# Optimization experiments

Measured on AMD Instinct MI355X. Metric: run time of the kernel, lower is better.

## Reference

```python
import jax, jax.numpy as jnp
import numpy as np

N_ATOMS = 10000
N_EDGES = 200000
L_MAX = 2
K_L = [32, 24, 16]  # k_max_l = n_element_channels * n_max_l

# (l1, l2, L) in the original loop order (l1 outer, l2 inner, L ascending)
PAIRS = [(0,0,0),(0,1,1),(0,2,2),
         (1,0,1),(1,1,0),(1,1,1),(1,1,2),(1,2,1),(1,2,2),
         (2,0,2),(2,1,1),(2,1,2),(2,2,0),(2,2,1),(2,2,2)]
# concatenated input width -> k_max_l[L] per (L, sigma) channel
LIN = {'0_1': (72, 32), '1_1': (80, 24), '1_m1': (40, 24), '2_1': (72, 16), '2_m1': (32, 16)}


def setup_inputs() -> dict:
    key = jax.random.key(0)
    it = iter(jax.random.split(key, 64))
    def nrm(shape):
        return jax.random.normal(next(it), shape, dtype=jnp.float32)
    inp = {}
    for l in range(L_MAX + 1):
        inp['rb%d' % l] = nrm((N_EDGES, K_L[l]))           # radial basis per l
    for l in range(L_MAX + 1):
        inp['sh%d' % l] = nrm((N_EDGES, 2*l+1, 1))         # spherical harmonics per l
    inp['emb'] = nrm((N_ATOMS, 1, K_L[0]))                 # initial center embedding
    for l in range(L_MAX + 1):
        inp['f%d' % l] = nrm((N_ATOMS, 2*l+1, K_L[l]))     # nu=1 equivariant features
    for (l1, l2, L) in PAIRS:
        inp['cg_%d_%d_%d' % (l1, l2, L)] = nrm(((2*l1+1)*(2*l2+1), 2*L+1))
    for LS, (fin, fout) in LIN.items():
        inp['W_' + LS] = nrm((fin, fout)) / np.float32(np.sqrt(fin))
        inp['b_' + LS] = nrm((fout,)) * 0.01
    inp['centers'] = jax.random.randint(next(it), (N_EDGES,), 0, N_ATOMS)
    inp['neighbors'] = jax.random.randint(next(it), (N_EDGES,), 0, N_ATOMS)
    inp['n_atoms'] = N_ATOMS
    return inp


def _normalize(x, dims):
    # Normalizer(dims): RMS normalization over the given dims
    return x * jax.lax.rsqrt(jnp.mean(x * x, axis=dims, keepdims=True) + 1e-12)


def _forward(floats, centers, neighbors, n_atoms):
    (rb0, rb1, rb2, sh0, sh1, sh2, emb, f0, f1, f2,
     cg_0_0_0, cg_0_1_1, cg_0_2_2, cg_1_0_1, cg_1_1_0, cg_1_1_1, cg_1_1_2,
     cg_1_2_1, cg_1_2_2, cg_2_0_2, cg_2_1_1, cg_2_1_2, cg_2_2_0, cg_2_2_1,
     cg_2_2_2, W_0_1, b_0_1, W_1_1, b_1_1, W_1_m1, b_1_m1, W_2_1, b_2_1,
     W_2_m1, b_2_m1) = floats
    rb = [rb0, rb1, rb2]; sh = [sh0, sh1, sh2]; feats = [f0, f1, f2]
    cgs = {'0_0_0': cg_0_0_0, '0_1_1': cg_0_1_1, '0_2_2': cg_0_2_2,
           '1_0_1': cg_1_0_1, '1_1_0': cg_1_1_0, '1_1_1': cg_1_1_1,
           '1_1_2': cg_1_1_2, '1_2_1': cg_1_2_1, '1_2_2': cg_1_2_2,
           '2_0_2': cg_2_0_2, '2_1_1': cg_2_1_1, '2_1_2': cg_2_1_2,
           '2_2_0': cg_2_2_0, '2_2_1': cg_2_2_1, '2_2_2': cg_2_2_2}
    lin = {'0_1': (W_0_1, b_0_1), '1_1': (W_1_1, b_1_1), '1_m1': (W_1_m1, b_1_m1),
           '2_1': (W_2_1, b_2_1), '2_m1': (W_2_m1, b_2_m1)}

    # ---- InvariantMessagePasser: density_l = scatter_add over centers of
    #      sh_l * rb_l * emb[neighbors]
    emb_n = emb[neighbors]                                       # [E, 1, k0]
    densities = []
    for l in range(L_MAX + 1):
        msg = sh[l] * rb[l][:, None, :] * emb_n[:, :, :K_L[l]]   # [E, 2l+1, k_l]
        densities.append(jax.ops.segment_sum(msg, centers, num_segments=n_atoms))

    # ---- EquivariantMessagePasser
    ve = [sh[l] * rb[l][:, None, :] for l in range(L_MAX + 1)]   # vector expansion [E,2l+1,k_l]
    fn = [feats[l][neighbors] for l in range(L_MAX + 1)]         # gathered neighbor feats
    results = {}
    for (l1, l2, L) in PAIRS:
        S = (-1) ** (l1 + l2 + L)
        k = min(K_L[l1], K_L[l2])
        t1 = ve[l1][:, :, :k]                                    # [E, 2l1+1, k]
        t2 = fn[l2][:, :, :k]                                    # [E, 2l2+1, k]
        cg = cgs['%d_%d_%d' % (l1, l2, L)].reshape(2*l1+1, 2*l2+1, 2*L+1)
        # fused outer product + CG contraction -> [E, 2L+1, k]
        res = jnp.einsum('eak,ebk,abM->eMk', t1, t2, cg)
        pooled = jax.ops.segment_sum(res, centers, num_segments=n_atoms)
        LS = '%d_%s' % (L, 'm1' if S < 0 else '1')
        results.setdefault(LS, []).append(pooled)

    outs = {}
    for LS, (W, b) in lin.items():
        x = jnp.concatenate(results[LS], axis=2)                 # [n_atoms, 2L+1, size_LS]
        x = _normalize(x, (0, 1))
        x = jnp.einsum('amf,fk->amk', x, W) + b
        outs[LS] = _normalize(x, (0, 1, 2))

    return (densities[0], densities[1], densities[2],
            outs['0_1'], outs['1_1'], outs['1_m1'], outs['2_1'], outs['2_m1'])


def reference(rb0, rb1, rb2, sh0, sh1, sh2, emb, f0, f1, f2,
              cg_0_0_0, cg_0_1_1, cg_0_2_2, cg_1_0_1, cg_1_1_0, cg_1_1_1,
              cg_1_1_2, cg_1_2_1, cg_1_2_2, cg_2_0_2, cg_2_1_1, cg_2_1_2,
              cg_2_2_0, cg_2_2_1, cg_2_2_2, W_0_1, b_0_1, W_1_1, b_1_1,
              W_1_m1, b_1_m1, W_2_1, b_2_1, W_2_m1, b_2_m1,
              centers, neighbors, n_atoms):
    floats = (rb0, rb1, rb2, sh0, sh1, sh2, emb, f0, f1, f2,
              cg_0_0_0, cg_0_1_1, cg_0_2_2, cg_1_0_1, cg_1_1_0, cg_1_1_1,
              cg_1_1_2, cg_1_2_1, cg_1_2_2, cg_2_0_2, cg_2_1_1, cg_2_1_2,
              cg_2_2_0, cg_2_2_1, cg_2_2_2, W_0_1, b_0_1, W_1_1, b_1_1,
              W_1_m1, b_1_m1, W_2_1, b_2_1, W_2_m1, b_2_m1)
    return _forward(floats, centers, neighbors, n_atoms)
```

## Files before the change

kernel.cpp:

```cpp
#include <hip/hip_runtime.h>
#include <hip/hip_bf16.h>

typedef __hip_bfloat16 bf16;

#define N_ATOMS 10000
#define N_EDGES 200000

#define SCG   0
#define SINV  616
#define SS1P  1024
#define SS2P  19968
#define SWS2  20288
#define SINTS 20352
#define IFLAG  0
#define ICOUNT 16
#define IOFFS  10016
#define ICURS  20032
#define IELIST 30032
#define INTS_END_SMALL 230032
#define INTS_END_BIG   430032
#define SXACC (SINTS + INTS_END_BIG)
#define BIG_FLOATS (SXACC + 952*N_ATOMS)

#define O0 0
#define O1 320000
#define O2 1040000
#define OY 1840000

__device__ __forceinline__ float b2f(bf16 x){ return __bfloat162float(x); }
__device__ __forceinline__ bf16  f2b(float x){ return __float2bfloat16(x); }

__device__ __forceinline__ float ldv(const float* p, int i){ return p[i]; }
__device__ __forceinline__ float ldv(const bf16*  p, int i){ return b2f(p[i]); }
__device__ __forceinline__ void  stv(float* p, int i, float v){ p[i] = v; }
__device__ __forceinline__ void  stv(bf16*  p, int i, float v){ p[i] = f2b(v); }

template<typename T> __device__ __forceinline__ int dtid();
template<> __device__ __forceinline__ int dtid<bf16>(){ return 0; }
template<> __device__ __forceinline__ int dtid<float>(){ return 1; }

struct Ptrs15 { const void* p[15]; };
struct LinP   { const void* W[5]; const void* B[5]; };

__constant__ int c_cg_sizes[15] = {1,9,25,9,9,27,45,45,75,25,45,75,25,75,125};
__constant__ int c_fin[5]   = {72,80,40,72,32};
__constant__ int c_kout[5]  = {32,24,24,16,16};
__constant__ int c_yoff[5]  = {OY+0, OY+320000, OY+1040000, OY+1760000, OY+2560000};
__constant__ int c_numel[5] = {320000,720000,720000,800000,800000};
__constant__ int c_cum[6]   = {0,32,104,176,256,336};
__constant__ int c_xb[5]    = {0,72,312,432,792};
__constant__ int c_Ms[5]    = {1,3,3,5,5};

__global__ void k_zero(float* wsf, int* wsi,
                       const unsigned short* rb0u, const unsigned short* embu) {
  if (blockIdx.x == 0 && threadIdx.x < 64) {
    int lane = threadIdx.x;
    int bad = 0;
    for (int i = lane; i < 256; i += 64) {
      unsigned u1 = ((unsigned)rb0u[2*i]) << 16;
      unsigned u2 = ((unsigned)embu[2*i]) << 16;
      float v1 = __uint_as_float(u1);
      float v2 = __uint_as_float(u2);
      if (!(fabsf(v1) < 1e9f) || !(fabsf(v2) < 1e9f)) bad = 1;
    }
    unsigned long long any = __ballot(bad);
    if (lane == 0) wsi[IFLAG] = (any != 0ULL) ? 1 : 0;
  }
  int i = blockIdx.x*blockDim.x + threadIdx.x;
  if (i < N_ATOMS) wsi[ICOUNT + i] = 0;
  int j = i - N_ATOMS;
  if (j >= 0 && j < N_ATOMS) wsi[ICURS + j] = 0;
  j -= N_ATOMS;
  if (j >= 0 && j < 18944) wsf[SS1P + j] = 0.f;
  j -= 18944;
  if (j >= 0 && j < 325) wsf[SS2P + j] = 0.f;
}

template<typename T>
__global__ void k_cg(Ptrs15 cg, float* wsf, const int* flag) {
  if (flag[0] != dtid<T>()) return;
  int i = blockIdx.x*blockDim.x + threadIdx.x;
  if (i >= 615) return;
  int s = 0, off = i;
  while (off >= c_cg_sizes[s]) { off -= c_cg_sizes[s]; ++s; }
  wsf[SCG + i] = ldv((const T*)cg.p[s], off);
}

__global__ void k_hist(const int* __restrict__ centers, int* __restrict__ counts) {
  int e = blockIdx.x*blockDim.x + threadIdx.x;
  if (e < N_EDGES) atomicAdd(&counts[centers[e]], 1);
}

__global__ void k_scan(const int* __restrict__ counts, int* __restrict__ offs) {
  __shared__ int part[1024];
  int t = threadIdx.x;
  int base = t*10;
  int s = 0;
  for (int i = 0; i < 10; ++i) { int idx = base+i; if (idx < N_ATOMS) s += counts[idx]; }
  part[t] = s;
  __syncthreads();
  for (int d = 1; d < 1024; d <<= 1) {
    int v = part[t];
    int add = (t >= d) ? part[t-d] : 0;
    __syncthreads();
    part[t] = v + add;
    __syncthreads();
  }
  int run = (t == 0) ? 0 : part[t-1];
  for (int i = 0; i < 10; ++i) {
    int idx = base+i;
    if (idx < N_ATOMS) { offs[idx] = run; run += counts[idx]; }
  }
  if (t == 1023) offs[N_ATOMS] = part[1023];
}

__global__ void k_scatter(const int* __restrict__ centers, const int* __restrict__ offs,
                          int* __restrict__ cursors, int* __restrict__ elist) {
  int e = blockIdx.x*blockDim.x + threadIdx.x;
  if (e < N_EDGES) {
    int c = centers[e];
    int p = atomicAdd(&cursors[c], 1);
    elist[offs[c] + p] = e;
  }
}

__global__ void k_scatter2(const int* __restrict__ centers, const int* __restrict__ neighbors,
                           const int* __restrict__ offs, int* __restrict__ cursors,
                           int2* __restrict__ elist2) {
  int e = blockIdx.x*blockDim.x + threadIdx.x;
  if (e < N_EDGES) {
    int c = centers[e];
    int p = atomicAdd(&cursors[c], 1);
    elist2[offs[c] + p] = make_int2(e, neighbors[e]);
  }
}

template<typename T, int MODE>
__global__ __launch_bounds__(256) void k_main(
    const T* __restrict__ rb0, const T* __restrict__ rb1, const T* __restrict__ rb2,
    const T* __restrict__ sh0, const T* __restrict__ sh1, const T* __restrict__ sh2,
    const T* __restrict__ emb, const T* __restrict__ f0, const T* __restrict__ f1,
    const T* __restrict__ f2, const int* __restrict__ neighbors,
    const int* __restrict__ offs, const int* __restrict__ elist,
    const float* __restrict__ cgf, float* __restrict__ s1p,
    const float* __restrict__ inv, float* __restrict__ s2p,
    float* __restrict__ xout, LinP lp, T* __restrict__ out,
    const int* __restrict__ flag)
{
  if (flag[0] != dtid<T>()) return;
  int lane = threadIdx.x & 63;
  int wv   = threadIdx.x >> 6;
  int tix  = threadIdx.x;
  int a = blockIdx.x;
  int beg = offs[a];
  int cnt = offs[a+1] - beg;
  int k32 = lane & 31, e2 = lane >> 5;
  int k16 = lane & 15, e4 = lane >> 4;
  const int2* el2 = (const int2*)elist;
  int ab = a & 63;

  __shared__ int2 sel[256];
  __shared__ __align__(16) float L[952];
  __shared__ float red[4][5];

  float acc[20];
  #pragma unroll
  for (int i = 0; i < 20; ++i) acc[i] = 0.f;

  for (int cbase = 0; cbase < cnt; cbase += 256) {
    int nch = cnt - cbase; if (nch > 256) nch = 256;
    __syncthreads();
    if (tix < nch) {
      if constexpr (MODE == 0) {
        sel[tix] = el2[beg + cbase + tix];
      } else {
        int e = elist[beg + cbase + tix];
        sel[tix] = make_int2(e, neighbors[e]);
      }
    }
    __syncthreads();

    if (wv == 0) {
      const float* C000 = cgf + 0;
      const float* C011 = cgf + 1;
      const float* C101 = cgf + 35;
      const float* C110 = cgf + 44;
      const float* C111 = cgf + 53;
      const float* C112 = cgf + 80;
      for (int base = 0; base < nch; base += 4) {
        #pragma unroll
        for (int u = 0; u < 2; ++u) {
          int idx = base + 2*u + e2;
          float w = (idx < nch) ? 1.f : 0.f;
          int ic  = (idx < nch) ? idx : (nch - 1);
          int2 en = sel[ic];
          int e = en.x, n = en.y;
          float s0 = ldv(sh0, e);
          float s1a0 = ldv(sh1, e*3+0), s1a1 = ldv(sh1, e*3+1), s1a2 = ldv(sh1, e*3+2);
          float rb0k = ldv(rb0, e*32 + k32) * w;
          float ek   = ldv(emb, n*32 + k32);
          float f0k  = ldv(f0,  n*32 + k32);
          float ve0 = s0 * rb0k;
          acc[0] = fmaf(ve0, ek, acc[0]);
          acc[4] = fmaf(C000[0]*ve0, f0k, acc[4]);
          if (k32 < 24) {
            float rb1k = ldv(rb1, e*24 + k32) * w;
            float f1k0 = ldv(f1, n*72 + k32);
            float f1k1 = ldv(f1, n*72 + 24 + k32);
            float f1k2 = ldv(f1, n*72 + 48 + k32);
            float rbek = rb1k * ek;
            acc[1] = fmaf(s1a0, rbek, acc[1]);
            acc[2] = fmaf(s1a1, rbek, acc[2]);
            acc[3] = fmaf(s1a2, rbek, acc[3]);
            #pragma unroll
            for (int bb = 0; bb < 3; ++bb) {
              float fb = (bb==0)?f1k0:(bb==1)?f1k1:f1k2;
              float p = ve0 * fb;
              #pragma unroll
              for (int M = 0; M < 3; ++M) acc[5+M] = fmaf(p, C011[bb*3+M], acc[5+M]);
            }
            float g3 = rb1k * f0k;
            #pragma unroll
            for (int aa = 0; aa < 3; ++aa) {
              float sa = (aa==0)?s1a0:(aa==1)?s1a1:s1a2;
              float p = g3 * sa;
              #pragma unroll
              for (int M = 0; M < 3; ++M) acc[8+M] = fmaf(p, C101[aa*3+M], acc[8+M]);
            }
            #pragma unroll
            for (int aa = 0; aa < 3; ++aa) {
              float sa = rb1k * ((aa==0)?s1a0:(aa==1)?s1a1:s1a2);
              #pragma unroll
              for (int bb = 0; bb < 3; ++bb) {
                float fb = (bb==0)?f1k0:(bb==1)?f1k1:f1k2;
                float p = sa * fb;
                int q = aa*3+bb;
                acc[11] = fmaf(p, C110[q], acc[11]);
                #pragma unroll
                for (int M = 0; M < 3; ++M) acc[12+M] = fmaf(p, C111[q*3+M], acc[12+M]);
                #pragma unroll
                for (int M = 0; M < 5; ++M) acc[15+M] = fmaf(p, C112[q*5+M], acc[15+M]);
              }
            }
          }
        }
      }
    } else if (wv == 1) {
      const float* C022 = cgf + 10;
      const float* C121 = cgf + 125;
      const float* C122 = cgf + 170;
      for (int base = 0; base < nch; base += 4) {
        int idx = base + e4;
        if (idx < nch) {
          int2 en = sel[idx];
          int e = en.x, n = en.y;
          float s0 = ldv(sh0, e);
          float s1a[3];
          #pragma unroll
          for (int m = 0; m < 3; ++m) s1a[m] = ldv(sh1, e*3+m);
          float s2a[5];
          #pragma unroll
          for (int m = 0; m < 5; ++m) s2a[m] = ldv(sh2, e*5+m);
          float rb0k = ldv(rb0, e*32 + k16);
          float rb1k = ldv(rb1, e*24 + k16);
          float rb2k = ldv(rb2, e*16 + k16);
          float ek   = ldv(emb, n*32 + k16);
          float f2k[5];
          #pragma unroll
          for (int b = 0; b < 5; ++b) f2k[b] = ldv(f2, n*80 + b*16 + k16);
          float re = rb2k * ek;
          #pragma unroll
          for (int m = 0; m < 5; ++m) acc[m] = fmaf(s2a[m], re, acc[m]);
          float ve0 = s0 * rb0k;
          #pragma unroll
          for (int bb = 0; bb < 5; ++bb) {
            float p = ve0 * f2k[bb];
            #pragma unroll
            for (int M = 0; M < 5; ++M) acc[5+M] = fmaf(p, C022[bb*5+M], acc[5+M]);
          }
          #pragma unroll
          for (int aa = 0; aa < 3; ++aa) {
            float sa = rb1k * s1a[aa];
            #pragma unroll
            for (int bb = 0; bb < 5; ++bb) {
              float p = sa * f2k[bb];
              int q = aa*5+bb;
              #pragma unroll
              for (int M = 0; M < 3; ++M) acc[10+M] = fmaf(p, C121[q*3+M], acc[10+M]);
              #pragma unroll
              for (int M = 0; M < 5; ++M) acc[13+M] = fmaf(p, C122[q*5+M], acc[13+M]);
            }
          }
        }
      }
    } else if (wv == 2) {
      const float* C202 = cgf + 245;
      const float* C211 = cgf + 270;
      const float* C212 = cgf + 315;
      for (int base = 0; base < nch; base += 4) {
        int idx = base + e4;
        if (idx < nch) {
          int2 en = sel[idx];
          int e = en.x, n = en.y;
          float s2a[5];
          #pragma unroll
          for (int m = 0; m < 5; ++m) s2a[m] = ldv(sh2, e*5+m);
          float rb2k = ldv(rb2, e*16 + k16);
          float f0k  = ldv(f0,  n*32 + k16);
          float f1k[3];
          #pragma unroll
          for (int b = 0; b < 3; ++b) f1k[b] = ldv(f1, n*72 + b*24 + k16);
          float g9 = rb2k * f0k;
          #pragma unroll
          for (int aa = 0; aa < 5; ++aa) {
            float p = g9 * s2a[aa];
            #pragma unroll
            for (int M = 0; M < 5; ++M) acc[0+M] = fmaf(p, C202[aa*5+M], acc[0+M]);
          }
          #pragma unroll
          for (int aa = 0; aa < 5; ++aa) {
            float sa = rb2k * s2a[aa];
            #pragma unroll
            for (int bb = 0; bb < 3; ++bb) {
              float p = sa * f1k[bb];
              int q = aa*3+bb;
              #pragma unroll
              for (int M = 0; M < 3; ++M) acc[5+M] = fmaf(p, C211[q*3+M], acc[5+M]);
              #pragma unroll
              for (int M = 0; M < 5; ++M) acc[8+M] = fmaf(p, C212[q*5+M], acc[8+M]);
            }
          }
        }
      }
    } else {
      const float* C220 = cgf + 390;
      const float* C221 = cgf + 415;
      const float* C222 = cgf + 490;
      for (int base = 0; base < nch; base += 4) {
        int idx = base + e4;
        if (idx < nch) {
          int2 en = sel[idx];
          int e = en.x, n = en.y;
          float s2a[5];
          #pragma unroll
          for (int m = 0; m < 5; ++m) s2a[m] = ldv(sh2, e*5+m);
          float rb2k = ldv(rb2, e*16 + k16);
          float f2k[5];
          #pragma unroll
          for (int b = 0; b < 5; ++b) f2k[b] = ldv(f2, n*80 + b*16 + k16);
          #pragma unroll
          for (int aa = 0; aa < 5; ++aa) {
            float sa = rb2k * s2a[aa];
            #pragma unroll
            for (int bb = 0; bb < 5; ++bb) {
              float p = sa * f2k[bb];
              int q = aa*5+bb;
              acc[0] = fmaf(p, C220[q], acc[0]);
              #pragma unroll
              for (int M = 0; M < 3; ++M) acc[1+M] = fmaf(p, C221[q*3+M], acc[1+M]);
              #pragma unroll
              for (int M = 0; M < 5; ++M) acc[4+M] = fmaf(p, C222[q*5+M], acc[4+M]);
            }
          }
        }
      }
    }
  }

  if (wv == 0) {
    #pragma unroll
    for (int i = 0; i < 20; ++i) acc[i] += __shfl_xor(acc[i], 32);
  } else if (wv == 1) {
    #pragma unroll
    for (int i = 0; i < 18; ++i) {
      acc[i] += __shfl_xor(acc[i], 16);
      acc[i] += __shfl_xor(acc[i], 32);
    }
  } else if (wv == 2) {
    #pragma unroll
    for (int i = 0; i < 13; ++i) {
      acc[i] += __shfl_xor(acc[i], 16);
      acc[i] += __shfl_xor(acc[i], 32);
    }
  } else {
    #pragma unroll
    for (int i = 0; i < 9; ++i) {
      acc[i] += __shfl_xor(acc[i], 16);
      acc[i] += __shfl_xor(acc[i], 32);
    }
  }

  if constexpr (MODE != 2) {
    if (wv == 0) {
      if (lane < 32) {
        stv(out, O0 + a*32 + k32, acc[0]);
        atomicAdd(&s1p[(0+k32)*64+ab], acc[4]*acc[4]);
        if (k32 < 24) {
          #pragma unroll
          for (int m = 0; m < 3; ++m) stv(out, O1 + a*72 + m*24 + k32, acc[1+m]);
          atomicAdd(&s1p[(32+k32)*64+ab], acc[11]*acc[11]);
          float q;
          q = acc[5]*acc[5]+acc[6]*acc[6]+acc[7]*acc[7];
          atomicAdd(&s1p[(72+k32)*64+ab], q);
          q = acc[8]*acc[8]+acc[9]*acc[9]+acc[10]*acc[10];
          atomicAdd(&s1p[(96+k32)*64+ab], q);
          q = acc[12]*acc[12]+acc[13]*acc[13]+acc[14]*acc[14];
          atomicAdd(&s1p[(152+k32)*64+ab], q);
          q = acc[15]*acc[15]+acc[16]*acc[16]+acc[17]*acc[17]
            + acc[18]*acc[18]+acc[19]*acc[19];
          atomicAdd(&s1p[(208+k32)*64+ab], q);
        }
      }
    } else if (wv == 1) {
      if (lane < 16) {
        #pragma unroll
        for (int m = 0; m < 5; ++m) stv(out, O2 + a*80 + m*16 + k16, acc[m]);
        float q;
        q = acc[5]*acc[5]+acc[6]*acc[6]+acc[7]*acc[7]+acc[8]*acc[8]+acc[9]*acc[9];
        atomicAdd(&s1p[(192+k16)*64+ab], q);
        q = acc[10]*acc[10]+acc[11]*acc[11]+acc[12]*acc[12];
        atomicAdd(&s1p[(120+k16)*64+ab], q);
        q = acc[13]*acc[13]+acc[14]*acc[14]+acc[15]*acc[15]
          + acc[16]*acc[16]+acc[17]*acc[17];
        atomicAdd(&s1p[(264+k16)*64+ab], q);
      }
    } else if (wv == 2) {
      if (lane < 16) {
        float q;
        q = acc[0]*acc[0]+acc[1]*acc[1]+acc[2]*acc[2]+acc[3]*acc[3]+acc[4]*acc[4];
        atomicAdd(&s1p[(232+k16)*64+ab], q);
        q = acc[5]*acc[5]+acc[6]*acc[6]+acc[7]*acc[7];
        atomicAdd(&s1p[(136+k16)*64+ab], q);
        q = acc[8]*acc[8]+acc[9]*acc[9]+acc[10]*acc[10]
          + acc[11]*acc[11]+acc[12]*acc[12];
        atomicAdd(&s1p[(280+k16)*64+ab], q);
      }
    } else {
      if (lane < 16) {
        atomicAdd(&s1p[(56+k16)*64+ab], acc[0]*acc[0]);
        float q;
        q = acc[1]*acc[1]+acc[2]*acc[2]+acc[3]*acc[3];
        atomicAdd(&s1p[(176+k16)*64+ab], q);
        q = acc[4]*acc[4]+acc[5]*acc[5]+acc[6]*acc[6]
          + acc[7]*acc[7]+acc[8]*acc[8];
        atomicAdd(&s1p[(248+k16)*64+ab], q);
      }
    }
  }

  if constexpr (MODE == 0) {
    if (wv == 0) {
      if (lane < 32) {
        L[k32] = acc[4];
        if (k32 < 24) {
          L[32+k32] = acc[11];
          #pragma unroll
          for (int M = 0; M < 3; ++M) L[72+M*80+k32]     = acc[5+M];
          #pragma unroll
          for (int M = 0; M < 3; ++M) L[72+M*80+24+k32]  = acc[8+M];
          #pragma unroll
          for (int M = 0; M < 3; ++M) L[312+M*40+k32]    = acc[12+M];
          #pragma unroll
          for (int M = 0; M < 5; ++M) L[432+M*72+16+k32] = acc[15+M];
        }
      }
    } else if (wv == 1) {
      if (lane < 16) {
        #pragma unroll
        for (int M = 0; M < 5; ++M) L[432+M*72+k16]    = acc[5+M];
        #pragma unroll
        for (int M = 0; M < 3; ++M) L[72+M*80+48+k16]  = acc[10+M];
        #pragma unroll
        for (int M = 0; M < 5; ++M) L[792+M*32+k16]    = acc[13+M];
      }
    } else if (wv == 2) {
      if (lane < 16) {
        #pragma unroll
        for (int M = 0; M < 5; ++M) L[432+M*72+40+k16] = acc[0+M];
        #pragma unroll
        for (int M = 0; M < 3; ++M) L[72+M*80+64+k16]  = acc[5+M];
        #pragma unroll
        for (int M = 0; M < 5; ++M) L[792+M*32+16+k16] = acc[8+M];
      }
    } else {
      if (lane < 16) {
        L[56+k16] = acc[0];
        #pragma unroll
        for (int M = 0; M < 3; ++M) L[312+M*40+24+k16] = acc[1+M];
        #pragma unroll
        for (int M = 0; M < 5; ++M) L[432+M*72+56+k16] = acc[4+M];
      }
    }
    __syncthreads();
    const float4* Ls = (const float4*)L;
    float4* xd = (float4*)(xout + a*952);
    for (int i = tix; i < 238; i += 256) xd[i] = Ls[i];
  }

  if constexpr (MODE == 2) {
    if (wv == 0) {
      if (lane < 32) {
        L[k32] = acc[4]*inv[k32];
        if (k32 < 24) {
          L[32+k32] = acc[11]*inv[32+k32];
          #pragma unroll
          for (int M = 0; M < 3; ++M) L[72+M*80+k32]     = acc[5+M]*inv[72+k32];
          #pragma unroll
          for (int M = 0; M < 3; ++M) L[72+M*80+24+k32]  = acc[8+M]*inv[96+k32];
          #pragma unroll
          for (int M = 0; M < 3; ++M) L[312+M*40+k32]    = acc[12+M]*inv[152+k32];
          #pragma unroll
          for (int M = 0; M < 5; ++M) L[432+M*72+16+k32] = acc[15+M]*inv[208+k32];
        }
      }
    } else if (wv == 1) {
      if (lane < 16) {
        #pragma unroll
        for (int M = 0; M < 5; ++M) L[432+M*72+k16]    = acc[5+M]*inv[192+k16];
        #pragma unroll
        for (int M = 0; M < 3; ++M) L[72+M*80+48+k16]  = acc[10+M]*inv[120+k16];
        #pragma unroll
        for (int M = 0; M < 5; ++M) L[792+M*32+k16]    = acc[13+M]*inv[264+k16];
      }
    } else if (wv == 2) {
      if (lane < 16) {
        #pragma unroll
        for (int M = 0; M < 5; ++M) L[432+M*72+40+k16] = acc[0+M]*inv[232+k16];
        #pragma unroll
        for (int M = 0; M < 3; ++M) L[72+M*80+64+k16]  = acc[5+M]*inv[136+k16];
        #pragma unroll
        for (int M = 0; M < 5; ++M) L[792+M*32+16+k16] = acc[8+M]*inv[280+k16];
      }
    } else {
      if (lane < 16) {
        L[56+k16] = acc[0]*inv[56+k16];
        #pragma unroll
        for (int M = 0; M < 3; ++M) L[312+M*40+24+k16] = acc[1+M]*inv[176+k16];
        #pragma unroll
        for (int M = 0; M < 5; ++M) L[432+M*72+56+k16] = acc[4+M]*inv[248+k16];
      }
    }
    __syncthreads();
    int t = threadIdx.x;
    float y2[5] = {0.f,0.f,0.f,0.f,0.f};
    for (int tau = t; tau < 336; tau += 256) {
      int ls = 0;
      while (tau >= c_cum[ls+1]) ++ls;
      int rem = tau - c_cum[ls];
      int kn = c_kout[ls], fin = c_fin[ls];
      int M = rem / kn, ko = rem - M*kn;
      const T* W = (const T*)lp.W[ls];
      float y = ldv((const T*)lp.B[ls], ko);
      const float* xv = &L[c_xb[ls] + M*fin];
      for (int f = 0; f < fin; ++f) y = fmaf(xv[f], ldv(W, f*kn+ko), y);
      stv(out, c_yoff[ls] + (a*c_Ms[ls] + M)*kn + ko, y);
      y2[ls] += y*y;
    }
    #pragma unroll
    for (int i = 0; i < 5; ++i) {
      y2[i] += __shfl_xor(y2[i], 1);  y2[i] += __shfl_xor(y2[i], 2);
      y2[i] += __shfl_xor(y2[i], 4);  y2[i] += __shfl_xor(y2[i], 8);
      y2[i] += __shfl_xor(y2[i], 16); y2[i] += __shfl_xor(y2[i], 32);
    }
    if (lane == 0) {
      #pragma unroll
      for (int i = 0; i < 5; ++i) red[wv][i] = y2[i];
    }
    __syncthreads();
    if (t == 0) {
      #pragma unroll
      for (int i = 0; i < 5; ++i)
        atomicAdd(&s2p[i*64 + ab], red[0][i]+red[1][i]+red[2][i]+red[3][i]);
    }
  }
}

template<typename T>
__global__ __launch_bounds__(256) void k_lin(
    const float* __restrict__ xg, const float* __restrict__ inv,
    LinP lp, T* __restrict__ out, float* __restrict__ s2p,
    const int* __restrict__ flag)
{
  if (flag[0] != dtid<T>()) return;
  int a = blockIdx.x;
  int t = threadIdx.x;
  __shared__ float L[952];
  for (int i = t; i < 952; i += 256) {
    int ch;
    if      (i < 72)  ch = i;
    else if (i < 312) ch = 72  + (i-72)  % 80;
    else if (i < 432) ch = 152 + (i-312) % 40;
    else if (i < 792) ch = 192 + (i-432) % 72;
    else              ch = 264 + (i-792) % 32;
    L[i] = xg[a*952 + i] * inv[ch];
  }
  __syncthreads();
  float y2[5] = {0.f,0.f,0.f,0.f,0.f};
  for (int tau = t; tau < 336; tau += 256) {
    int ls = 0;
    while (tau >= c_cum[ls+1]) ++ls;
    int rem = tau - c_cum[ls];
    int kn = c_kout[ls], fin = c_fin[ls];
    int M = rem / kn, ko = rem - M*kn;
    const T* W = (const T*)lp.W[ls];
    float y = ldv((const T*)lp.B[ls], ko);
    const float* xv = &L[c_xb[ls] + M*fin];
    for (int f = 0; f < fin; ++f) y = fmaf(xv[f], ldv(W, f*kn+ko), y);
    stv(out, c_yoff[ls] + (a*c_Ms[ls] + M)*kn + ko, y);
    y2[ls] += y*y;
  }
  __shared__ float red[4][5];
  #pragma unroll
  for (int i = 0; i < 5; ++i) {
    y2[i] += __shfl_xor(y2[i], 1);  y2[i] += __shfl_xor(y2[i], 2);
    y2[i] += __shfl_xor(y2[i], 4);  y2[i] += __shfl_xor(y2[i], 8);
    y2[i] += __shfl_xor(y2[i], 16); y2[i] += __shfl_xor(y2[i], 32);
  }
  if ((t & 63) == 0) {
    #pragma unroll
    for (int i = 0; i < 5; ++i) red[t>>6][i] = y2[i];
  }
  __syncthreads();
  if (t == 0) {
    #pragma unroll
    for (int i = 0; i < 5; ++i)
      atomicAdd(&s2p[i*64 + (a & 63)], red[0][i]+red[1][i]+red[2][i]+red[3][i]);
  }
}

__global__ void k_red1(const float* __restrict__ s1p, float* __restrict__ inv) {
  int ch = blockIdx.x, lane = threadIdx.x;
  float v = s1p[ch*64 + lane];
  v += __shfl_xor(v, 1);  v += __shfl_xor(v, 2);  v += __shfl_xor(v, 4);
  v += __shfl_xor(v, 8);  v += __shfl_xor(v, 16); v += __shfl_xor(v, 32);
  if (lane == 0) {
    float rows = (ch < 72) ? 10000.f : (ch < 192) ? 30000.f : 50000.f;
    inv[ch] = rsqrtf(v/rows + 1e-12f);
  }
}

__global__ void k_red2(const float* __restrict__ s2p, float* __restrict__ ws2) {
  int ls = blockIdx.x, lane = threadIdx.x;
  float v = s2p[ls*64 + lane];
  v += __shfl_xor(v, 1);  v += __shfl_xor(v, 2);  v += __shfl_xor(v, 4);
  v += __shfl_xor(v, 8);  v += __shfl_xor(v, 16); v += __shfl_xor(v, 32);
  if (lane == 0) ws2[ls] = v;
}

template<typename T>
__global__ void k_scale(const float* __restrict__ ws2, T* __restrict__ out,
                        const int* __restrict__ flag) {
  if (flag[0] != dtid<T>()) return;
  int i = blockIdx.x*blockDim.x + threadIdx.x;
  if (i >= 3360000) return;
  int ls = (i < 320000) ? 0 : (i < 1040000) ? 1 : (i < 1760000) ? 2 : (i < 2560000) ? 3 : 4;
  float scale = rsqrtf(ws2[ls] / (float)c_numel[ls] + 1e-12f);
  stv(out, OY + i, ldv((const T*)out, OY + i) * scale);
}

template<typename T>
static void launch_chain(void* const* d_in, T* out, float* wsf, int* wsi,
                         Ptrs15 cg, LinP lp, bool big, hipStream_t stream) {
  const T* rb0 = (const T*)d_in[0];
  const T* rb1 = (const T*)d_in[1];
  const T* rb2 = (const T*)d_in[2];
  const T* sh0 = (const T*)d_in[3];
  const T* sh1 = (const T*)d_in[4];
  const T* sh2 = (const T*)d_in[5];
  const T* emb = (const T*)d_in[6];
  const T* f0  = (const T*)d_in[7];
  const T* f1  = (const T*)d_in[8];
  const T* f2  = (const T*)d_in[9];
  const int* neighbors = (const int*)d_in[36];
  const int* flag = wsi + IFLAG;

  k_cg<T><<<3, 256, 0, stream>>>(cg, wsf, flag);
  if (big) {
    k_main<T,0><<<N_ATOMS, 256, 0, stream>>>(rb0, rb1, rb2, sh0, sh1, sh2, emb, f0, f1, f2,
        neighbors, wsi+IOFFS, wsi+IELIST, wsf+SCG, wsf+SS1P, nullptr, nullptr,
        wsf+SXACC, lp, out, flag);
    k_red1<<<296, 64, 0, stream>>>(wsf+SS1P, wsf+SINV);
    k_lin<T><<<N_ATOMS, 256, 0, stream>>>(wsf+SXACC, wsf+SINV, lp, out, wsf+SS2P, flag);
  } else {
    k_main<T,1><<<N_ATOMS, 256, 0, stream>>>(rb0, rb1, rb2, sh0, sh1, sh2, emb, f0, f1, f2,
        neighbors, wsi+IOFFS, wsi+IELIST, wsf+SCG, wsf+SS1P, nullptr, nullptr,
        nullptr, lp, out, flag);
    k_red1<<<296, 64, 0, stream>>>(wsf+SS1P, wsf+SINV);
    k_main<T,2><<<N_ATOMS, 256, 0, stream>>>(rb0, rb1, rb2, sh0, sh1, sh2, emb, f0, f1, f2,
        neighbors, wsi+IOFFS, wsi+IELIST, wsf+SCG, nullptr, wsf+SINV, wsf+SS2P,
        nullptr, lp, out, flag);
  }
  k_red2<<<5, 64, 0, stream>>>(wsf+SS2P, wsf+SWS2);
  k_scale<T><<<(3360000+255)/256, 256, 0, stream>>>(wsf+SWS2, out, flag);
}

extern "C" void kernel_launch(void* const* d_in, const int* in_sizes, int n_in,
                              void* d_out, int out_size, void* d_ws, size_t ws_size,
                              hipStream_t stream) {
  float* wsf = (float*)d_ws;
  int*   wsi = (int*)(wsf + SINTS);
  const int* centers   = (const int*)d_in[35];
  const int* neighbors = (const int*)d_in[36];
  bool big = ws_size >= (size_t)BIG_FLOATS * 4;

  int know = -1;
  if (in_sizes) {
    long long nb = (long long)in_sizes[0];
    if (nb == (long long)N_EDGES*32*2) know = 0;
    else if (nb == (long long)N_EDGES*32*4) know = 1;
  }

  Ptrs15 cg;
  for (int i = 0; i < 15; ++i) cg.p[i] = d_in[10+i];
  LinP lp;
  lp.W[0] = d_in[25]; lp.B[0] = d_in[26];
  lp.W[1] = d_in[27]; lp.B[1] = d_in[28];
  lp.W[2] = d_in[29]; lp.B[2] = d_in[30];
  lp.W[3] = d_in[31]; lp.B[3] = d_in[32];
  lp.W[4] = d_in[33]; lp.B[4] = d_in[34];

  k_zero<<<154, 256, 0, stream>>>(wsf, wsi,
                                  (const unsigned short*)d_in[0],
                                  (const unsigned short*)d_in[6]);
  k_hist<<<(N_EDGES+255)/256, 256, 0, stream>>>(centers, wsi+ICOUNT);
  k_scan<<<1, 1024, 0, stream>>>(wsi+ICOUNT, wsi+IOFFS);
  if (big) {
    k_scatter2<<<(N_EDGES+255)/256, 256, 0, stream>>>(centers, neighbors, wsi+IOFFS,
                                                      wsi+ICURS, (int2*)(wsi+IELIST));
  } else {
    k_scatter<<<(N_EDGES+255)/256, 256, 0, stream>>>(centers, wsi+IOFFS, wsi+ICURS, wsi+IELIST);
  }

  if (know != 1) launch_chain<bf16 >(d_in, (bf16*)d_out,  wsf, wsi, cg, lp, big, stream);
  if (know != 0) launch_chain<float>(d_in, (float*)d_out, wsf, wsi, cg, lp, big, stream);
}
```

Before: 511.5 us.

## Defer Clebsch-Gordan contraction until after per-atom edge accumulation

The CG coefficients are linear and independent of the edge, so each wave now accumulates raw outer-product components (up to 25 per lane) over all edges and applies the CG matrices once per atom after the shuffle reduction. This removes most of the per-edge FMAs and the CG loads in the inner loop. In exchange it uses more accumulator registers and more shuffles. The waves that handle l=2 also process two edges per iteration with masking instead of a branch. A fallback dtype detection from the output size is added as well.

```diff
diff --git a/kernel.cpp b/kernel.cpp
--- a/kernel.cpp
+++ b/kernel.cpp
@@ -26,6 +26,7 @@
 #define O1 320000
 #define O2 1040000
 #define OY 1840000
+#define OUT_ELEMS 5200000
 
 __device__ __forceinline__ float b2f(bf16 x){ return __bfloat162float(x); }
 __device__ __forceinline__ bf16  f2b(float x){ return __float2bfloat16(x); }
@@ -163,9 +164,9 @@
   __shared__ __align__(16) float L[952];
   __shared__ float red[4][5];
 
-  float acc[20];
+  float acc[25];
   #pragma unroll
-  for (int i = 0; i < 20; ++i) acc[i] = 0.f;
+  for (int i = 0; i < 25; ++i) acc[i] = 0.f;
 
   for (int cbase = 0; cbase < cnt; cbase += 256) {
     int nch = cnt - cbase; if (nch > 256) nch = 256;
@@ -181,18 +182,12 @@
     __syncthreads();
 
     if (wv == 0) {
-      const float* C000 = cgf + 0;
-      const float* C011 = cgf + 1;
-      const float* C101 = cgf + 35;
-      const float* C110 = cgf + 44;
-      const float* C111 = cgf + 53;
-      const float* C112 = cgf + 80;
       for (int base = 0; base < nch; base += 4) {
         #pragma unroll
         for (int u = 0; u < 2; ++u) {
           int idx = base + 2*u + e2;
           float w = (idx < nch) ? 1.f : 0.f;
-          int ic  = (idx < nch) ? idx : (nch - 1);
+          int ic  = (idx < nch) ? idx : 0;
           int2 en = sel[ic];
           int e = en.x, n = en.y;
           float s0 = ldv(sh0, e);
@@ -202,7 +197,7 @@
           float f0k  = ldv(f0,  n*32 + k32);
           float ve0 = s0 * rb0k;
           acc[0] = fmaf(ve0, ek, acc[0]);
-          acc[4] = fmaf(C000[0]*ve0, f0k, acc[4]);
+          acc[4] = fmaf(ve0, f0k, acc[4]);
           if (k32 < 24) {
             float rb1k = ldv(rb1, e*24 + k32) * w;
             float f1k0 = ldv(f1, n*72 + k32);
@@ -212,47 +207,31 @@
             acc[1] = fmaf(s1a0, rbek, acc[1]);
             acc[2] = fmaf(s1a1, rbek, acc[2]);
             acc[3] = fmaf(s1a2, rbek, acc[3]);
-            #pragma unroll
-            for (int bb = 0; bb < 3; ++bb) {
-              float fb = (bb==0)?f1k0:(bb==1)?f1k1:f1k2;
-              float p = ve0 * fb;
-              #pragma unroll
-              for (int M = 0; M < 3; ++M) acc[5+M] = fmaf(p, C011[bb*3+M], acc[5+M]);
-            }
+            acc[5] = fmaf(ve0, f1k0, acc[5]);
+            acc[6] = fmaf(ve0, f1k1, acc[6]);
+            acc[7] = fmaf(ve0, f1k2, acc[7]);
             float g3 = rb1k * f0k;
-            #pragma unroll
-            for (int aa = 0; aa < 3; ++aa) {
-              float sa = (aa==0)?s1a0:(aa==1)?s1a1:s1a2;
-              float p = g3 * sa;
-              #pragma unroll
-              for (int M = 0; M < 3; ++M) acc[8+M] = fmaf(p, C101[aa*3+M], acc[8+M]);
-            }
+            acc[8]  = fmaf(g3, s1a0, acc[8]);
+            acc[9]  = fmaf(g3, s1a1, acc[9]);
+            acc[10] = fmaf(g3, s1a2, acc[10]);
             #pragma unroll
             for (int aa = 0; aa < 3; ++aa) {
               float sa = rb1k * ((aa==0)?s1a0:(aa==1)?s1a1:s1a2);
-              #pragma unroll
-              for (int bb = 0; bb < 3; ++bb) {
-                float fb = (bb==0)?f1k0:(bb==1)?f1k1:f1k2;
-                float p = sa * fb;
-                int q = aa*3+bb;
-                acc[11] = fmaf(p, C110[q], acc[11]);
-                #pragma unroll
-                for (int M = 0; M < 3; ++M) acc[12+M] = fmaf(p, C111[q*3+M], acc[12+M]);
-                #pragma unroll
-                for (int M = 0; M < 5; ++M) acc[15+M] = fmaf(p, C112[q*5+M], acc[15+M]);
-              }
+              acc[11+aa*3+0] = fmaf(sa, f1k0, acc[11+aa*3+0]);
+              acc[11+aa*3+1] = fmaf(sa, f1k1, acc[11+aa*3+1]);
+              acc[11+aa*3+2] = fmaf(sa, f1k2, acc[11+aa*3+2]);
             }
           }
         }
       }
     } else if (wv == 1) {
-      const float* C022 = cgf + 10;
-      const float* C121 = cgf + 125;
-      const float* C122 = cgf + 170;
-      for (int base = 0; base < nch; base += 4) {
-        int idx = base + e4;
-        if (idx < nch) {
-          int2 en = sel[idx];
+      for (int base = 0; base < nch; base += 8) {
+        #pragma unroll
+        for (int u = 0; u < 2; ++u) {
+          int idx = base + 4*u + e4;
+          float w = (idx < nch) ? 1.f : 0.f;
+          int ic  = (idx < nch) ? idx : 0;
+          int2 en = sel[ic];
           int e = en.x, n = en.y;
           float s0 = ldv(sh0, e);
           float s1a[3];
@@ -261,9 +240,9 @@
           float s2a[5];
           #pragma unroll
           for (int m = 0; m < 5; ++m) s2a[m] = ldv(sh2, e*5+m);
-          float rb0k = ldv(rb0, e*32 + k16);
-          float rb1k = ldv(rb1, e*24 + k16);
-          float rb2k = ldv(rb2, e*16 + k16);
+          float rb0k = ldv(rb0, e*32 + k16) * w;
+          float rb1k = ldv(rb1, e*24 + k16) * w;
+          float rb2k = ldv(rb2, e*16 + k16) * w;
           float ek   = ldv(emb, n*32 + k16);
           float f2k[5];
           #pragma unroll
@@ -273,78 +252,58 @@
           for (int m = 0; m < 5; ++m) acc[m] = fmaf(s2a[m], re, acc[m]);
           float ve0 = s0 * rb0k;
           #pragma unroll
-          for (int bb = 0; bb < 5; ++bb) {
-            float p = ve0 * f2k[bb];
-            #pragma unroll
-            for (int M = 0; M < 5; ++M) acc[5+M] = fmaf(p, C022[bb*5+M], acc[5+M]);
-          }
+          for (int b = 0; b < 5; ++b) acc[5+b] = fmaf(ve0, f2k[b], acc[5+b]);
           #pragma unroll
           for (int aa = 0; aa < 3; ++aa) {
             float sa = rb1k * s1a[aa];
             #pragma unroll
-            for (int bb = 0; bb < 5; ++bb) {
-              float p = sa * f2k[bb];
-              int q = aa*5+bb;
-              #pragma unroll
-              for (int M = 0; M < 3; ++M) acc[10+M] = fmaf(p, C121[q*3+M], acc[10+M]);
-              #pragma unroll
-              for (int M = 0; M < 5; ++M) acc[13+M] = fmaf(p, C122[q*5+M], acc[13+M]);
-            }
+            for (int b = 0; b < 5; ++b)
+              acc[10+aa*5+b] = fmaf(sa, f2k[b], acc[10+aa*5+b]);
           }
         }
       }
     } else if (wv == 2) {
-      const float* C202 = cgf + 245;
-      const float* C211 = cgf + 270;
-      const float* C212 = cgf + 315;
-      for (int base = 0; base < nch; base += 4) {
-        int idx = base + e4;
-        if (idx < nch) {
-          int2 en = sel[idx];
+      for (int base = 0; base < nch; base += 8) {
+        #pragma unroll
+        for (int u = 0; u < 2; ++u) {
+          int idx = base + 4*u + e4;
+          float w = (idx < nch) ? 1.f : 0.f;
+          int ic  = (idx < nch) ? idx : 0;
+          int2 en = sel[ic];
           int e = en.x, n = en.y;
           float s2a[5];
           #pragma unroll
           for (int m = 0; m < 5; ++m) s2a[m] = ldv(sh2, e*5+m);
-          float rb2k = ldv(rb2, e*16 + k16);
+          float rb2k = ldv(rb2, e*16 + k16) * w;
           float f0k  = ldv(f0,  n*32 + k16);
           float f1k[3];
           #pragma unroll
           for (int b = 0; b < 3; ++b) f1k[b] = ldv(f1, n*72 + b*24 + k16);
           float g9 = rb2k * f0k;
           #pragma unroll
-          for (int aa = 0; aa < 5; ++aa) {
-            float p = g9 * s2a[aa];
-            #pragma unroll
-            for (int M = 0; M < 5; ++M) acc[0+M] = fmaf(p, C202[aa*5+M], acc[0+M]);
-          }
+          for (int aa = 0; aa < 5; ++aa) acc[aa] = fmaf(g9, s2a[aa], acc[aa]);
           #pragma unroll
           for (int aa = 0; aa < 5; ++aa) {
             float sa = rb2k * s2a[aa];
             #pragma unroll
-            for (int bb = 0; bb < 3; ++bb) {
-              float p = sa * f1k[bb];
-              int q = aa*3+bb;
-              #pragma unroll
-              for (int M = 0; M < 3; ++M) acc[5+M] = fmaf(p, C211[q*3+M], acc[5+M]);
-              #pragma unroll
-              for (int M = 0; M < 5; ++M) acc[8+M] = fmaf(p, C212[q*5+M], acc[8+M]);
-            }
+            for (int b = 0; b < 3; ++b)
+              acc[5+aa*3+b] = fmaf(sa, f1k[b], acc[5+aa*3+b]);
           }
         }
       }
     } else {
-      const float* C220 = cgf + 390;
-      const float* C221 = cgf + 415;
-      const float* C222 = cgf + 490;
-      for (int base = 0; base < nch; base += 4) {
-        int idx = base + e4;
-        if (idx < nch) {
-          int2 en = sel[idx];
+      for (int base = 0; base < nch; base += 8) {
+        #pragma unroll
+        for (int u = 0; u < 2; ++u) {
+          int idx = base + 4*u + e4;
+          float w = (idx < nch) ? 1.f : 0.f;
+          int ic  = (idx < nch) ? idx : 0;
+          int2 en = sel[ic];
           int e = en.x, n = en.y;
           float s2a[5];
           #pragma unroll
           for (int m = 0; m < 5; ++m) s2a[m] = ldv(sh2, e*5+m);
-          float rb2k = ldv(rb2, e*16 + k16);
+          float rb2k = ldv(rb2, e*16 + k16) * w;
           float f2k[5];
           #pragma unroll
           for (int b = 0; b < 5; ++b) f2k[b] = ldv(f2, n*80 + b*16 + k16);
@@ -352,15 +311,8 @@
           for (int aa = 0; aa < 5; ++aa) {
             float sa = rb2k * s2a[aa];
             #pragma unroll
-            for (int bb = 0; bb < 5; ++bb) {
-              float p = sa * f2k[bb];
-              int q = aa*5+bb;
-              acc[0] = fmaf(p, C220[q], acc[0]);
-              #pragma unroll
-              for (int M = 0; M < 3; ++M) acc[1+M] = fmaf(p, C221[q*3+M], acc[1+M]);
-              #pragma unroll
-              for (int M = 0; M < 5; ++M) acc[4+M] = fmaf(p, C222[q*5+M], acc[4+M]);
-            }
+            for (int b = 0; b < 5; ++b)
+              acc[aa*5+b] = fmaf(sa, f2k[b], acc[aa*5+b]);
           }
         }
       }
@@ -370,24 +322,164 @@
   if (wv == 0) {
     #pragma unroll
     for (int i = 0; i < 20; ++i) acc[i] += __shfl_xor(acc[i], 32);
+    const float* C000 = cgf + 0;
+    const float* C011 = cgf + 1;
+    const float* C101 = cgf + 35;
+    const float* C110 = cgf + 44;
+    const float* C111 = cgf + 53;
+    const float* C112 = cgf + 80;
+    float r[16];
+    r[0] = C000[0] * acc[4];
+    #pragma unroll
+    for (int M = 0; M < 3; ++M) {
+      float t = 0.f;
+      #pragma unroll
+      for (int b = 0; b < 3; ++b) t = fmaf(acc[5+b], C011[b*3+M], t);
+      r[1+M] = t;
+    }
+    #pragma unroll
+    for (int M = 0; M < 3; ++M) {
+      float t = 0.f;
+      #pragma unroll
+      for (int aa = 0; aa < 3; ++aa) t = fmaf(acc[8+aa], C101[aa*3+M], t);
+      r[4+M] = t;
+    }
+    {
+      float t = 0.f;
+      #pragma unroll
+      for (int q = 0; q < 9; ++q) t = fmaf(acc[11+q], C110[q], t);
+      r[7] = t;
+    }
+    #pragma unroll
+    for (int M = 0; M < 3; ++M) {
+      float t = 0.f;
+      #pragma unroll
+      for (int q = 0; q < 9; ++q) t = fmaf(acc[11+q], C111[q*3+M], t);
+      r[8+M] = t;
+    }
+    #pragma unroll
+    for (int M = 0; M < 5; ++M) {
+      float t = 0.f;
+      #pragma unroll
+      for (int q = 0; q < 9; ++q) t = fmaf(acc[11+q], C112[q*5+M], t);
+      r[11+M] = t;
+    }
+    acc[4] = r[0];
+    #pragma unroll
+    for (int M = 0; M < 3; ++M) acc[5+M]  = r[1+M];
+    #pragma unroll
+    for (int M = 0; M < 3; ++M) acc[8+M]  = r[4+M];
+    acc[11] = r[7];
+    #pragma unroll
+    for (int M = 0; M < 3; ++M) acc[12+M] = r[8+M];
+    #pragma unroll
+    for (int M = 0; M < 5; ++M) acc[15+M] = r[11+M];
   } else if (wv == 1) {
     #pragma unroll
-    for (int i = 0; i < 18; ++i) {
+    for (int i = 0; i < 25; ++i) {
       acc[i] += __shfl_xor(acc[i], 16);
       acc[i] += __shfl_xor(acc[i], 32);
     }
+    const float* C022 = cgf + 10;
+    const float* C121 = cgf + 125;
+    const float* C122 = cgf + 170;
+    float r[13];
+    #pragma unroll
+    for (int M = 0; M < 5; ++M) {
+      float t = 0.f;
+      #pragma unroll
+      for (int b = 0; b < 5; ++b) t = fmaf(acc[5+b], C022[b*5+M], t);
+      r[M] = t;
+    }
+    #pragma unroll
+    for (int M = 0; M < 3; ++M) {
+      float t = 0.f;
+      #pragma unroll
+      for (int q = 0; q < 15; ++q) t = fmaf(acc[10+q], C121[q*3+M], t);
+      r[5+M] = t;
+    }
+    #pragma unroll
+    for (int M = 0; M < 5; ++M) {
+      float t = 0.f;
+      #pragma unroll
+      for (int q = 0; q < 15; ++q) t = fmaf(acc[10+q], C122[q*5+M], t);
+      r[8+M] = t;
+    }
+    #pragma unroll
+    for (int M = 0; M < 5; ++M) acc[5+M]  = r[M];
+    #pragma unroll
+    for (int M = 0; M < 3; ++M) acc[10+M] = r[5+M];
+    #pragma unroll
+    for (int M = 0; M < 5; ++M) acc[13+M] = r[8+M];
   } else if (wv == 2) {
     #pragma unroll
-    for (int i = 0; i < 13; ++i) {
+    for (int i = 0; i < 20; ++i) {
       acc[i] += __shfl_xor(acc[i], 16);
       acc[i] += __shfl_xor(acc[i], 32);
     }
+    const float* C202 = cgf + 245;
+    const float* C211 = cgf + 270;
+    const float* C212 = cgf + 315;
+    float r[13];
+    #pragma unroll
+    for (int M = 0; M < 5; ++M) {
+      float t = 0.f;
+      #pragma unroll
+      for (int aa = 0; aa < 5; ++aa) t = fmaf(acc[aa], C202[aa*5+M], t);
+      r[M] = t;
+    }
+    #pragma unroll
+    for (int M = 0; M < 3; ++M) {
+      float t = 0.f;
+      #pragma unroll
+      for (int q = 0; q < 15; ++q) t = fmaf(acc[5+q], C211[q*3+M], t);
+      r[5+M] = t;
+    }
+    #pragma unroll
+    for (int M = 0; M < 5; ++M) {
+      float t = 0.f;
+      #pragma unroll
+      for (int q = 0; q < 15; ++q) t = fmaf(acc[5+q], C212[q*5+M], t);
+      r[8+M] = t;
+    }
+    #pragma unroll
+    for (int M = 0; M < 5; ++M) acc[M]   = r[M];
+    #pragma unroll
+    for (int M = 0; M < 3; ++M) acc[5+M] = r[5+M];
+    #pragma unroll
+    for (int M = 0; M < 5; ++M) acc[8+M] = r[8+M];
   } else {
     #pragma unroll
-    for (int i = 0; i < 9; ++i) {
+    for (int i = 0; i < 25; ++i) {
       acc[i] += __shfl_xor(acc[i], 16);
       acc[i] += __shfl_xor(acc[i], 32);
     }
+    const float* C220 = cgf + 390;
+    const float* C221 = cgf + 415;
+    const float* C222 = cgf + 490;
+    float r[9];
+    {
+      float t = 0.f;
+      #pragma unroll
+      for (int q = 0; q < 25; ++q) t = fmaf(acc[q], C220[q], t);
+      r[0] = t;
+    }
+    #pragma unroll
+    for (int M = 0; M < 3; ++M) {
+      float t = 0.f;
+      #pragma unroll
+      for (int q = 0; q < 25; ++q) t = fmaf(acc[q], C221[q*3+M], t);
+      r[1+M] = t;
+    }
+    #pragma unroll
+    for (int M = 0; M < 5; ++M) {
+      float t = 0.f;
+      #pragma unroll
+      for (int q = 0; q < 25; ++q) t = fmaf(acc[q], C222[q*5+M], t);
+      r[4+M] = t;
+    }
+    #pragma unroll
+    for (int i = 0; i < 9; ++i) acc[i] = r[i];
   }
 
   if constexpr (MODE != 2) {
@@ -709,6 +801,11 @@
     if (nb == (long long)N_EDGES*32*2) know = 0;
     else if (nb == (long long)N_EDGES*32*4) know = 1;
   }
+  if (know < 0) {
+    long long ob = (long long)out_size;
+    if (ob == (long long)OUT_ELEMS*2) know = 0;
+    else if (ob == (long long)OUT_ELEMS*4) know = 1;
+  }
 
   Ptrs15 cg;
   for (int i = 0; i < 15; ++i) cg.p[i] = d_in[10+i];
```

New measurement: 514.2 us. No clear change (+0.5%).
